# Performance work log

Measured on AMD Instinct MI355X. Metric: run time of the kernel, lower is better.

Reference implementation:

```python
import jax, jax.numpy as jnp
import numpy as np

N = 4096          # patch_dim**2, patch_dim=64
F_IN = 44         # pre_Nfeat = Nfeat/3
F_OUT = 44
K = 16            # min_nn - 8
RANK = 11         # rank_theta


def setup_inputs() -> dict:
    key = jax.random.key(0)
    ks = jax.random.split(key, 6)
    return {
        "h": jax.random.normal(ks[0], (1, N, F_IN), jnp.float32),
        "local_mask": jnp.ones((N, N), jnp.float32),
        "W_lab": jax.random.normal(ks[1], (F_IN, F_IN), jnp.float32) * (1.0 / np.sqrt(F_IN)),
        "b_lab": jax.random.normal(ks[2], (1, F_IN), jnp.float32) * 0.1,
        "W_th1": jax.random.normal(ks[3], (F_IN, F_IN * RANK), jnp.float32) * (1.0 / F_IN),
        "b_th1": jnp.zeros((1, RANK, F_IN), jnp.float32),
        "W_th2": jax.random.normal(ks[4], (F_IN, F_OUT * RANK), jnp.float32) * (1.0 / F_IN),
        "b_th2": jnp.zeros((1, RANK, F_OUT), jnp.float32),
        "W_thl": jax.random.normal(ks[5], (F_IN, RANK), jnp.float32) * (1.0 / np.sqrt(RANK)),
        "b_thl": jnp.zeros((1, RANK), jnp.float32),
    }


def reference(h, local_mask, W_lab, b_lab, W_th1, b_th1, W_th2, b_th2, W_thl, b_thl):
    # --- compute_graph: pairwise sq. distances, masked, self-dist forced minimal ---
    hh = h[0]                                        # [N, F]
    hg = jax.lax.stop_gradient(hh)                   # torch detaches h for the graph
    sq = jnp.sum(hg * hg, axis=-1)                   # [N]
    D = jnp.abs(sq[:, None] + sq[None, :] - 2.0 * (hg @ hg.T))
    D = D * local_mask - 2.0 * jnp.eye(N, dtype=D.dtype)
    # --- kNN: 25 smallest distances; keep ranks 9..24 as neighbors, rank 0 = self ---
    _, top_idx = jax.lax.top_k(-D, K + 9)            # [N, 25]
    nbr_idx = top_idx[:, 9:].reshape(-1)             # [N*K] node-major edge order
    ctr_idx = jnp.repeat(top_idx[:, 0], K)           # [N*K]
    # --- gather (irregular access, the kernel target) ---
    x_tilde1 = hh[nbr_idx]                           # [E, F] neighbor features
    x_tilde2 = hh[ctr_idx]                           # [E, F] center features
    labels = x_tilde1 - x_tilde2                     # [E, F]
    d_labels = jnp.sum(labels * labels, axis=-1).reshape(N, K)
    # --- edge-conditioned low-rank filter generation ---
    lab = jax.nn.leaky_relu(labels @ W_lab + b_lab, negative_slope=0.2)  # [E, F]
    theta1 = (lab @ W_th1).reshape(-1, RANK, F_IN) + b_th1               # [E, R, F]
    theta2 = (lab @ W_th2).reshape(-1, RANK, F_OUT) + b_th2              # [E, R, Fo]
    thetal = lab @ W_thl + b_thl                                         # [E, R]
    t = jnp.einsum('erf,ef->er', theta1, x_tilde1) * thetal              # [E, R]
    x = jnp.einsum('erf,er->ef', theta2, t)                              # [E, Fo]
    # --- distance-weighted mean over K neighbors (scatter-mean) ---
    x = x.reshape(N, K, F_OUT) * jnp.exp(-d_labels / 10.0)[:, :, None]
    x = jnp.mean(x, axis=1)
    return x.reshape(1, N, F_OUT)
```

## Files before the change

### kernel.cpp

```cpp
#include <hip/hip_runtime.h>
#include <float.h>

#define N 4096
#define FI 44
#define RK 11
#define KNN 16
#define NSEL 25
#define NROW 4
#define ME 496

typedef unsigned long long u64;
typedef unsigned int u32;

__global__ __launch_bounds__(256) void k_prep_all(const float* __restrict__ h,
                                                  float* __restrict__ sq,
                                                  float* __restrict__ hT,
                                                  const float* __restrict__ W1,
                                                  const float* __restrict__ b1,
                                                  const float* __restrict__ W2,
                                                  const float* __restrict__ b2,
                                                  float* __restrict__ P1e,
                                                  float* __restrict__ W2T4) {
  const int tid = threadIdx.x;
  if (blockIdx.x < 16) {
    int n = blockIdx.x * 256 + tid;
    const float4* hr = reinterpret_cast<const float4*>(h + (size_t)n * FI);
    float v[FI];
    float s = 0.f;
#pragma unroll
    for (int c4 = 0; c4 < 11; c4++) {
      float4 x = hr[c4];
      v[4*c4] = x.x; v[4*c4+1] = x.y; v[4*c4+2] = x.z; v[4*c4+3] = x.w;
      s += x.x*x.x + x.y*x.y + x.z*x.z + x.w*x.w;
    }
    sq[n] = s;
#pragma unroll
    for (int c = 0; c < FI; c++) hT[c * N + n] = v[c];
  } else if (blockIdx.x < 272) {
    const int grp = tid >> 6, lane = tid & 63;
    const int nb = (blockIdx.x - 16) * 16 + grp * 4;
    const float4* h4 = reinterpret_cast<const float4*>(h);
    float4 hq[4][11];
#pragma unroll
    for (int q = 0; q < 4; q++)
#pragma unroll
      for (int c4 = 0; c4 < 11; c4++)
        hq[q][c4] = h4[(size_t)(nb + q) * 11 + c4];
#pragma unroll
    for (int i = 0; i < 8; i++) {
      int m = lane + 64 * i;
      if (m < 495) {
        const float4* wrow = reinterpret_cast<const float4*>(
            (m < 484) ? W1 + (size_t)(m % FI) * 484 + (m / FI) * FI
                      : b1 + (size_t)(m - 484) * FI);
        float a0 = 0.f, a1 = 0.f, a2 = 0.f, a3 = 0.f;
#pragma unroll
        for (int c4 = 0; c4 < 11; c4++) {
          float4 wv = wrow[c4];
          a0 += wv.x*hq[0][c4].x + wv.y*hq[0][c4].y + wv.z*hq[0][c4].z + wv.w*hq[0][c4].w;
          a1 += wv.x*hq[1][c4].x + wv.y*hq[1][c4].y + wv.z*hq[1][c4].z + wv.w*hq[1][c4].w;
          a2 += wv.x*hq[2][c4].x + wv.y*hq[2][c4].y + wv.z*hq[2][c4].z + wv.w*hq[2][c4].w;
          a3 += wv.x*hq[3][c4].x + wv.y*hq[3][c4].y + wv.z*hq[3][c4].z + wv.w*hq[3][c4].w;
        }
        P1e[(size_t)(nb + 0) * ME + m] = a0;
        P1e[(size_t)(nb + 1) * ME + m] = a1;
        P1e[(size_t)(nb + 2) * ME + m] = a2;
        P1e[(size_t)(nb + 3) * ME + m] = a3;
      }
    }
  } else {
    int idx0 = (blockIdx.x - 272) * 256 + tid;
    for (int idx = idx0; idx < 496 * 64; idx += 16 * 256) {
      int mc = idx >> 8;
      int fo = (idx >> 2) & 63;
      int i  = idx & 3;
      int m  = 4 * mc + i;
      float v = 0.f;
      if (fo < FI && m < 495) {
        if (m < 484) { int c = m % FI, r = m / FI; v = W2[c * 484 + r * FI + fo]; }
        else         { v = b2[(m - 484) * FI + fo]; }
      }
      W2T4[idx] = v;
    }
  }
}

__global__ __launch_bounds__(512) void k_dist_topk(const float* __restrict__ hT,
                                                   const float* __restrict__ sq,
                                                   const float* __restrict__ mask,
                                                   int* __restrict__ ctr_idx,
                                                   int* __restrict__ nbr_idx) {
  __shared__ __align__(16) float hi[NROW][FI];
  __shared__ float sqi4[NROW];
  __shared__ u32 lmin[NROW][512];
  __shared__ u32 Tsh[NROW];
  __shared__ int cnts[NROW];
  __shared__ u64 cbuf[NROW][128];
  const int tid = threadIdx.x;
  const int r0 = blockIdx.x * NROW;

  if (tid < NROW) { cnts[tid] = 0; sqi4[tid] = sq[r0 + tid]; }
  for (int t = tid; t < NROW * FI; t += 512) {
    int rr = t / FI, c = t % FI;
    hi[rr][c] = hT[c * N + (r0 + rr)];
  }
  __syncthreads();

  const float4* sq4p = reinterpret_cast<const float4*>(sq);
  const float4* mask4 = reinterpret_cast<const float4*>(mask);
  float4 m4r[2][NROW];
  float4 sq4r[2];
#pragma unroll
  for (int s = 0; s < 2; s++) {
    sq4r[s] = sq4p[s * 512 + tid];
#pragma unroll
    for (int rr = 0; rr < NROW; rr++)
      m4r[s][rr] = mask4[(size_t)(r0 + rr) * 1024 + s * 512 + tid];
  }

  const float4* hT4 = reinterpret_cast<const float4*>(hT);
  float4 acc[NROW][2];
#pragma unroll
  for (int rr = 0; rr < NROW; rr++)
#pragma unroll
    for (int s = 0; s < 2; s++) acc[rr][s] = make_float4(0.f, 0.f, 0.f, 0.f);

#pragma unroll 4
  for (int c = 0; c < FI; c++) {
    float4 v0 = hT4[c * 1024 + tid];
    float4 v1 = hT4[c * 1024 + 512 + tid];
#pragma unroll
    for (int rr = 0; rr < NROW; rr++) {
      float hc = hi[rr][c];
      acc[rr][0].x += hc * v0.x; acc[rr][0].y += hc * v0.y;
      acc[rr][0].z += hc * v0.z; acc[rr][0].w += hc * v0.w;
      acc[rr][1].x += hc * v1.x; acc[rr][1].y += hc * v1.y;
      acc[rr][1].z += hc * v1.z; acc[rr][1].w += hc * v1.w;
    }
  }

  u32 key[NROW][8];
#pragma unroll
  for (int s = 0; s < 2; s++) {
    float4 sq4 = sq4r[s];
    int jb = s * 2048 + 4 * tid;
#pragma unroll
    for (int rr = 0; rr < NROW; rr++) {
      int row = r0 + rr;
      float4 m4 = m4r[s][rr];
      float sqr = sqi4[rr];
      float d0 = fabsf(sqr + sq4.x - 2.f * acc[rr][s].x) * m4.x;
      float d1 = fabsf(sqr + sq4.y - 2.f * acc[rr][s].y) * m4.y;
      float d2 = fabsf(sqr + sq4.z - 2.f * acc[rr][s].z) * m4.z;
      float d3 = fabsf(sqr + sq4.w - 2.f * acc[rr][s].w) * m4.w;
      d0 -= (jb + 0 == row) ? 2.f : 0.f;
      d1 -= (jb + 1 == row) ? 2.f : 0.f;
      d2 -= (jb + 2 == row) ? 2.f : 0.f;
      d3 -= (jb + 3 == row) ? 2.f : 0.f;
      u32 u0 = __float_as_uint(d0); u0 ^= (u32)((int)u0 >> 31) | 0x80000000u;
      u32 u1 = __float_as_uint(d1); u1 ^= (u32)((int)u1 >> 31) | 0x80000000u;
      u32 u2 = __float_as_uint(d2); u2 ^= (u32)((int)u2 >> 31) | 0x80000000u;
      u32 u3 = __float_as_uint(d3); u3 ^= (u32)((int)u3 >> 31) | 0x80000000u;
      key[rr][s * 4 + 0] = u0; key[rr][s * 4 + 1] = u1;
      key[rr][s * 4 + 2] = u2; key[rr][s * 4 + 3] = u3;
    }
  }

#pragma unroll
  for (int rr = 0; rr < NROW; rr++) {
    u32 m = key[rr][0];
#pragma unroll
    for (int i = 1; i < 8; i++) m = key[rr][i] < m ? key[rr][i] : m;
    lmin[rr][tid] = m;
  }
  __syncthreads();

  const int w = tid >> 6, lane = tid & 63;

  if (w < NROW) {
    u32 g = lmin[w][lane];
#pragma unroll
    for (int k = 1; k < 8; k++) {
      u32 x = lmin[w][64 * k + lane];
      g = x < g ? x : g;
    }
#pragma unroll
    for (int kk = 2; kk <= 64; kk <<= 1)
#pragma unroll
      for (int jj = kk >> 1; jj > 0; jj >>= 1) {
        u32 o = __shfl_xor(g, jj, 64);
        bool low = (lane & jj) == 0, asc = (lane & kk) == 0;
        u32 mn = o < g ? o : g, mx = o < g ? g : o;
        g = (low == asc) ? mn : mx;
      }
    if (lane == 24) Tsh[w] = g;
  }
  __syncthreads();

#pragma unroll
  for (int rr = 0; rr < NROW; rr++) {
    u32 Tr = Tsh[rr];
#pragma unroll
    for (int s = 0; s < 2; s++)
#pragma unroll
      for (int i = 0; i < 4; i++) {
        u32 kv = key[rr][s * 4 + i];
        if (kv <= Tr) {
          int p = atomicAdd(&cnts[rr], 1);
          if (p < 128) cbuf[rr][p] = ((u64)kv << 12) | (u64)(s * 2048 + 4 * tid + i);
        }
      }
  }
  __syncthreads();

  if (w < NROW) {
    const u64 UMAX = ~0ull;
    int cnt = cnts[w];
    u64 v0 = (lane < cnt) ? cbuf[w][lane] : UMAX;
    u64 v1 = (64 + lane < cnt) ? cbuf[w][64 + lane] : UMAX;
#pragma unroll
    for (int kk = 2; kk <= 128; kk <<= 1) {
#pragma unroll
      for (int jj = kk >> 1; jj > 0; jj >>= 1) {
        if (jj >= 64) {
          bool asc = (lane & kk) == 0;
          u64 mn = v0 < v1 ? v0 : v1, mx = v0 < v1 ? v1 : v0;
          v0 = asc ? mn : mx; v1 = asc ? mx : mn;
        } else {
          bool low = (lane & jj) == 0;
          bool asc0 = (lane & kk) == 0;
          bool asc1 = ((64 + lane) & kk) == 0;
          u64 o0 = __shfl_xor(v0, jj, 64);
          v0 = (low == asc0) ? (o0 < v0 ? o0 : v0) : (o0 < v0 ? v0 : o0);
          u64 o1 = __shfl_xor(v1, jj, 64);
          v1 = (low == asc1) ? (o1 < v1 ? o1 : v1) : (o1 < v1 ? v1 : o1);
        }
      }
    }
    int row = r0 + w;
    int idx = (int)(v0 & 4095ull);
    if (lane == 0) ctr_idx[row] = idx;
    if (lane >= 9 && lane < NSEL) nbr_idx[row * KNN + (lane - 9)] = idx;
  }
}

__global__ __launch_bounds__(256) void k_edge_out(
    const float* __restrict__ h,
    const int* __restrict__ ctr_idx, const int* __restrict__ nbr_idx,
    const float* __restrict__ W_lab, const float* __restrict__ b_lab,
    const float* __restrict__ Wl, const float* __restrict__ bl,
    const float* __restrict__ P1e,
    const float* __restrict__ W2T4,
    float* __restrict__ out)
{
  __shared__ __align__(16) float WlabT[FI][FI];
  __shared__ __align__(16) float lbl[64][FI];
  __shared__ __align__(16) float WlT[RK][FI];
  __shared__ __align__(16) float hcs[4][FI];
  __shared__ __align__(16) float GeL[4][ME];
  __shared__ __align__(16) float pacc[4][4][64];
  __shared__ float blabS[FI];
  __shared__ float blS[RK];
  __shared__ float tfs[64][12];
  __shared__ float wexpS[64];
  __shared__ int nbrL[64];
  __shared__ int ctrL[4];
  const int tid = threadIdx.x;
  const int b = blockIdx.x;
  const float4* h4 = reinterpret_cast<const float4*>(h);

  if (tid < 64) nbrL[tid] = nbr_idx[b * 64 + tid];
  if (tid < 4) ctrL[tid] = ctr_idx[b * 4 + tid];
  if (tid < RK) blS[tid] = bl[tid];
  if (tid >= 64 && tid < 64 + FI) blabS[tid - 64] = b_lab[tid - 64];
  for (int t = tid; t < FI * FI; t += 256) {
    int c = t / FI, f = t % FI;
    WlabT[f][c] = W_lab[t];
  }
  for (int t = tid; t < FI * RK; t += 256) {
    int c = t / RK, r = t % RK;
    WlT[r][c] = Wl[t];
  }
  __syncthreads();

  if (tid < 44) {
    int nn = tid / 11, c4 = tid % 11;
    *reinterpret_cast<float4*>(&hcs[nn][4 * c4]) = h4[(size_t)ctrL[nn] * 11 + c4];
  }
  __syncthreads();
  for (int t = tid; t < 64 * 11; t += 256) {
    int e = t / 11, c4 = t % 11;
    float4 hv = h4[(size_t)nbrL[e] * 11 + c4];
    float4 hc = *reinterpret_cast<const float4*>(&hcs[e >> 4][4 * c4]);
    float4 d;
    d.x = hv.x - hc.x; d.y = hv.y - hc.y; d.z = hv.z - hc.z; d.w = hv.w - hc.w;
    *reinterpret_cast<float4*>(&lbl[e][4 * c4]) = d;
  }
  __syncthreads();

  const int e = tid >> 2;
  const int g = tid & 3;

  float4 lbr[11];
#pragma unroll
  for (int c4 = 0; c4 < 11; c4++)
    lbr[c4] = *reinterpret_cast<const float4*>(&lbl[e][4 * c4]);
  if (g == 0) {
    float s = 0.f;
#pragma unroll
    for (int c4 = 0; c4 < 11; c4++)
      s += lbr[c4].x*lbr[c4].x + lbr[c4].y*lbr[c4].y + lbr[c4].z*lbr[c4].z + lbr[c4].w*lbr[c4].w;
    wexpS[e] = expf(-s * 0.1f) * (1.0f / 16.0f);
  }

  float la[11];
#pragma unroll
  for (int u = 0; u < 11; u++) {
    int f = g + 4 * u;
    float acc = blabS[f];
#pragma unroll
    for (int c4 = 0; c4 < 11; c4++) {
      float4 wv = *reinterpret_cast<const float4*>(&WlabT[f][4 * c4]);
      acc += wv.x*lbr[c4].x + wv.y*lbr[c4].y + wv.z*lbr[c4].z + wv.w*lbr[c4].w;
    }
    la[u] = acc >= 0.f ? acc : 0.2f * acc;
  }
  __syncthreads();
#pragma unroll
  for (int u = 0; u < 11; u++) lbl[e][g + 4 * u] = la[u];
  __syncthreads();

  {
#pragma unroll
    for (int c4 = 0; c4 < 11; c4++)
      lbr[c4] = *reinterpret_cast<const float4*>(&lbl[e][4 * c4]);
    const float* P1r = P1e + (size_t)nbrL[e] * ME;
    float wex = wexpS[e];
#pragma unroll
    for (int rr = 0; rr < 3; rr++) {
      int r = g + 4 * rr;
      if (r < RK) {
        float tp = 0.f, tlp = 0.f;
#pragma unroll
        for (int c4 = 0; c4 < 11; c4++) {
          float4 p4 = *reinterpret_cast<const float4*>(P1r + r * FI + 4 * c4);
          float4 w4 = *reinterpret_cast<const float4*>(&WlT[r][4 * c4]);
          float4 l4 = lbr[c4];
          tp  += l4.x*p4.x + l4.y*p4.y + l4.z*p4.z + l4.w*p4.w;
          tlp += l4.x*w4.x + l4.y*w4.y + l4.z*w4.z + l4.w*w4.w;
        }
        tfs[e][r] = (tp + P1r[484 + r]) * (tlp + blS[r]) * wex;
      }
    }
  }
  __syncthreads();

  const int nn = tid >> 6, lane = tid & 63;
  const int w = nn;
  if (lane < FI) {
    float acc2[RK];
#pragma unroll
    for (int r = 0; r < RK; r++) acc2[r] = 0.f;
    for (int k = 0; k < KNN; k++) {
      float lv = lbl[nn * 16 + k][lane];
#pragma unroll
      for (int r = 0; r < RK; r++) acc2[r] += lv * tfs[nn * 16 + k][r];
    }
#pragma unroll
    for (int r = 0; r < RK; r++) GeL[nn][r * FI + lane] = acc2[r];
  } else if (lane < FI + RK) {
    int r = lane - FI;
    float ss = 0.f;
    for (int k = 0; k < KNN; k++) ss += tfs[nn * 16 + k][r];
    GeL[nn][484 + r] = ss;
  } else if (lane == 55) {
    GeL[nn][495] = 0.f;
  }
  __syncthreads();

  {
    const float4* W2v = reinterpret_cast<const float4*>(W2T4);
    float a0 = 0.f, a1 = 0.f, a2 = 0.f, a3 = 0.f;
    for (int mc = w * 31; mc < (w + 1) * 31; mc++) {
      float4 wv = W2v[mc * 64 + lane];
      float4 g0 = *reinterpret_cast<const float4*>(&GeL[0][4 * mc]);
      float4 g1 = *reinterpret_cast<const float4*>(&GeL[1][4 * mc]);
      float4 g2 = *reinterpret_cast<const float4*>(&GeL[2][4 * mc]);
      float4 g3 = *reinterpret_cast<const float4*>(&GeL[3][4 * mc]);
      a0 += wv.x*g0.x + wv.y*g0.y + wv.z*g0.z + wv.w*g0.w;
      a1 += wv.x*g1.x + wv.y*g1.y + wv.z*g1.z + wv.w*g1.w;
      a2 += wv.x*g2.x + wv.y*g2.y + wv.z*g2.z + wv.w*g2.w;
      a3 += wv.x*g3.x + wv.y*g3.y + wv.z*g3.z + wv.w*g3.w;
    }
    pacc[w][0][lane] = a0;
    pacc[w][1][lane] = a1;
    pacc[w][2][lane] = a2;
    pacc[w][3][lane] = a3;
  }
  __syncthreads();

  if (tid < 4 * FI) {
    int n2 = tid / FI, fo = tid - (tid / FI) * FI;
    out[(size_t)(b * 4 + n2) * FI + fo] =
        pacc[0][n2][fo] + pacc[1][n2][fo] + pacc[2][n2][fo] + pacc[3][n2][fo];
  }
}

extern "C" void kernel_launch(void* const* d_in, const int* in_sizes, int n_in,
                              void* d_out, int out_size, void* d_ws, size_t ws_size,
                              hipStream_t stream) {
  const float* h     = (const float*)d_in[0];
  const float* mask  = (const float*)d_in[1];
  const float* W_lab = (const float*)d_in[2];
  const float* b_lab = (const float*)d_in[3];
  const float* W1    = (const float*)d_in[4];
  const float* b1    = (const float*)d_in[5];
  const float* W2    = (const float*)d_in[6];
  const float* b2    = (const float*)d_in[7];
  const float* Wl    = (const float*)d_in[8];
  const float* bl    = (const float*)d_in[9];

  float* sqw  = (float*)d_ws;
  float* hT   = sqw + N;
  int*   ctr  = (int*)(hT + (size_t)FI * N);
  int*   nbr  = ctr + N;
  float* P1e  = (float*)(nbr + N * KNN);
  float* W2T4 = P1e + (size_t)N * ME;

  k_prep_all<<<288, 256, 0, stream>>>(h, sqw, hT, W1, b1, W2, b2, P1e, W2T4);
  k_dist_topk<<<N / NROW, 512, 0, stream>>>(hT, sqw, mask, ctr, nbr);
  k_edge_out<<<N * KNN / 64, 256, 0, stream>>>(h, ctr, nbr, W_lab, b_lab, Wl, bl, P1e, W2T4, (float*)d_out);
}
```

Baseline: 97.40 us.

## Move P1 projection and W2 transpose into the distance/top-k kernel launch

```diff
diff --git a/kernel.cpp b/kernel.cpp
--- a/kernel.cpp
+++ b/kernel.cpp
@@ -8,69 +8,55 @@
 #define NSEL 25
 #define NROW 4
 #define ME 496
+#define DBLK (N / NROW)
+#define PBLK (N / 8)
 
 typedef unsigned long long u64;
 typedef unsigned int u32;
 
-__global__ __launch_bounds__(256) void k_prep_all(const float* __restrict__ h,
-                                                  float* __restrict__ sq,
-                                                  float* __restrict__ hT,
-                                                  const float* __restrict__ W1,
-                                                  const float* __restrict__ b1,
-                                                  const float* __restrict__ W2,
-                                                  const float* __restrict__ b2,
-                                                  float* __restrict__ P1e,
-                                                  float* __restrict__ W2T4) {
+__global__ __launch_bounds__(256) void k_prep(const float* __restrict__ h,
+                                              float* __restrict__ sq,
+                                              float* __restrict__ hT) {
   const int tid = threadIdx.x;
-  if (blockIdx.x < 16) {
-    int n = blockIdx.x * 256 + tid;
-    const float4* hr = reinterpret_cast<const float4*>(h + (size_t)n * FI);
-    float v[FI];
-    float s = 0.f;
-#pragma unroll
-    for (int c4 = 0; c4 < 11; c4++) {
-      float4 x = hr[c4];
-      v[4*c4] = x.x; v[4*c4+1] = x.y; v[4*c4+2] = x.z; v[4*c4+3] = x.w;
-      s += x.x*x.x + x.y*x.y + x.z*x.z + x.w*x.w;
-    }
-    sq[n] = s;
-#pragma unroll
-    for (int c = 0; c < FI; c++) hT[c * N + n] = v[c];
-  } else if (blockIdx.x < 272) {
-    const int grp = tid >> 6, lane = tid & 63;
-    const int nb = (blockIdx.x - 16) * 16 + grp * 4;
-    const float4* h4 = reinterpret_cast<const float4*>(h);
-    float4 hq[4][11];
-#pragma unroll
-    for (int q = 0; q < 4; q++)
-#pragma unroll
-      for (int c4 = 0; c4 < 11; c4++)
-        hq[q][c4] = h4[(size_t)(nb + q) * 11 + c4];
-#pragma unroll
-    for (int i = 0; i < 8; i++) {
-      int m = lane + 64 * i;
-      if (m < 495) {
-        const float4* wrow = reinterpret_cast<const float4*>(
-            (m < 484) ? W1 + (size_t)(m % FI) * 484 + (m / FI) * FI
-                      : b1 + (size_t)(m - 484) * FI);
-        float a0 = 0.f, a1 = 0.f, a2 = 0.f, a3 = 0.f;
-#pragma unroll
-        for (int c4 = 0; c4 < 11; c4++) {
-          float4 wv = wrow[c4];
-          a0 += wv.x*hq[0][c4].x + wv.y*hq[0][c4].y + wv.z*hq[0][c4].z + wv.w*hq[0][c4].w;
-          a1 += wv.x*hq[1][c4].x + wv.y*hq[1][c4].y + wv.z*hq[1][c4].z + wv.w*hq[1][c4].w;
-          a2 += wv.x*hq[2][c4].x + wv.y*hq[2][c4].y + wv.z*hq[2][c4].z + wv.w*hq[2][c4].w;
-          a3 += wv.x*hq[3][c4].x + wv.y*hq[3][c4].y + wv.z*hq[3][c4].z + wv.w*hq[3][c4].w;
-        }
-        P1e[(size_t)(nb + 0) * ME + m] = a0;
-        P1e[(size_t)(nb + 1) * ME + m] = a1;
-        P1e[(size_t)(nb + 2) * ME + m] = a2;
-        P1e[(size_t)(nb + 3) * ME + m] = a3;
-      }
-    }
-  } else {
-    int idx0 = (blockIdx.x - 272) * 256 + tid;
-    for (int idx = idx0; idx < 496 * 64; idx += 16 * 256) {
+  int n = blockIdx.x * 256 + tid;
+  const float4* hr = reinterpret_cast<const float4*>(h + (size_t)n * FI);
+  float v[FI];
+  float s = 0.f;
+#pragma unroll
+  for (int c4 = 0; c4 < 11; c4++) {
+    float4 x = hr[c4];
+    v[4*c4] = x.x; v[4*c4+1] = x.y; v[4*c4+2] = x.z; v[4*c4+3] = x.w;
+    s += x.x*x.x + x.y*x.y + x.z*x.z + x.w*x.w;
+  }
+  sq[n] = s;
+#pragma unroll
+  for (int c = 0; c < FI; c++) hT[c * N + n] = v[c];
+}
+
+__global__ __launch_bounds__(512) void k_dist_p1(const float* __restrict__ hT,
+                                                 const float* __restrict__ sq,
+                                                 const float* __restrict__ mask,
+                                                 int* __restrict__ ctr_idx,
+                                                 int* __restrict__ nbr_idx,
+                                                 const float* __restrict__ h,
+                                                 const float* __restrict__ W1,
+                                                 const float* __restrict__ b1,
+                                                 const float* __restrict__ W2,
+                                                 const float* __restrict__ b2,
+                                                 float* __restrict__ P1e,
+                                                 float* __restrict__ W2T4) {
+  __shared__ __align__(16) float hi[NROW][FI];
+  __shared__ float sqi4[NROW];
+  __shared__ u32 lmin[NROW][512];
+  __shared__ u32 Tsh[NROW];
+  __shared__ int cnts[NROW];
+  __shared__ u64 cbuf[NROW][128];
+  const int tid = threadIdx.x;
+  const int w = tid >> 6, lane = tid & 63;
+
+  if (blockIdx.x >= DBLK + PBLK) {
+    int idx0 = (blockIdx.x - DBLK - PBLK) * 512 + tid;
+    for (int idx = idx0; idx < 496 * 64; idx += 4 * 512) {
       int mc = idx >> 8;
       int fo = (idx >> 2) & 63;
       int i  = idx & 3;
@@ -82,21 +68,34 @@
       }
       W2T4[idx] = v;
     }
-  }
-}
-
-__global__ __launch_bounds__(512) void k_dist_topk(const float* __restrict__ hT,
-                                                   const float* __restrict__ sq,
-                                                   const float* __restrict__ mask,
-                                                   int* __restrict__ ctr_idx,
-                                                   int* __restrict__ nbr_idx) {
-  __shared__ __align__(16) float hi[NROW][FI];
-  __shared__ float sqi4[NROW];
-  __shared__ u32 lmin[NROW][512];
-  __shared__ u32 Tsh[NROW];
-  __shared__ int cnts[NROW];
-  __shared__ u64 cbuf[NROW][128];
-  const int tid = threadIdx.x;
+    return;
+  }
+  if (blockIdx.x >= DBLK) {
+    const int n = (blockIdx.x - DBLK) * 8 + w;
+    const float4* h4 = reinterpret_cast<const float4*>(h);
+    float4 hq[11];
+#pragma unroll
+    for (int c4 = 0; c4 < 11; c4++) hq[c4] = h4[(size_t)n * 11 + c4];
+    float* P1r = P1e + (size_t)n * ME;
+#pragma unroll
+    for (int i = 0; i < 8; i++) {
+      int m = lane + 64 * i;
+      if (m < 495) {
+        const float4* wrow = reinterpret_cast<const float4*>(
+            (m < 484) ? W1 + (size_t)(m % FI) * 484 + (m / FI) * FI
+                      : b1 + (size_t)(m - 484) * FI);
+        float a = 0.f;
+#pragma unroll
+        for (int c4 = 0; c4 < 11; c4++) {
+          float4 wv = wrow[c4];
+          a += wv.x*hq[c4].x + wv.y*hq[c4].y + wv.z*hq[c4].z + wv.w*hq[c4].w;
+        }
+        P1r[m] = a;
+      }
+    }
+    return;
+  }
+
   const int r0 = blockIdx.x * NROW;
 
   if (tid < NROW) { cnts[tid] = 0; sqi4[tid] = sq[r0 + tid]; }
@@ -174,8 +173,6 @@
     lmin[rr][tid] = m;
   }
   __syncthreads();
-
-  const int w = tid >> 6, lane = tid & 63;
 
   if (w < NROW) {
     u32 g = lmin[w][lane];
@@ -427,7 +424,8 @@
   float* P1e  = (float*)(nbr + N * KNN);
   float* W2T4 = P1e + (size_t)N * ME;
 
-  k_prep_all<<<288, 256, 0, stream>>>(h, sqw, hT, W1, b1, W2, b2, P1e, W2T4);
-  k_dist_topk<<<N / NROW, 512, 0, stream>>>(hT, sqw, mask, ctr, nbr);
+  k_prep<<<16, 256, 0, stream>>>(h, sqw, hT);
+  k_dist_p1<<<DBLK + PBLK + 4, 512, 0, stream>>>(hT, sqw, mask, ctr, nbr,
+                                                 h, W1, b1, W2, b2, P1e, W2T4);
   k_edge_out<<<N * KNN / 64, 256, 0, stream>>>(h, ctr, nbr, W_lab, b_lab, Wl, bl, P1e, W2T4, (float*)d_out);
 }
```

Measured after the change: 145.6 us. 49.5% more time.
